# Performance work log

Hardware: AMD Instinct MI355X
Metric: run time of the kernel (lower is better)

The kernel has to match this reference:

```python
import jax, jax.numpy as jnp
import numpy as np

N_ORDER = 256      # HiPPO order (window_size=[256])
OUT_LEN = 96       # output_window_size
IN_LEN = 720       # input_window_size
MULTISCALE = [1, 2, 4]
MODES = 32         # min(32, min(OUT_LEN, IN_LEN)//2)
EPS = 1e-5


def _transition(N):
    Q = np.arange(N, dtype=np.float64)
    R = (2 * Q + 1)[:, None]
    j, i = np.meshgrid(Q, Q)
    A = np.where(i < j, -1.0, (-1.0) ** (i - j + 1)) * R
    B = (-1.0) ** Q[:, None] * R
    return A, B


def _bilinear_discretize(A, B, dt):
    # scipy cont2discrete(method='bilinear'): Ad = (I - dt/2 A)^-1 (I + dt/2 A), Bd = (I - dt/2 A)^-1 dt B
    n = A.shape[0]
    I = np.eye(n)
    ima = I - 0.5 * dt * A
    Ad = np.linalg.solve(ima, I + 0.5 * dt * A)
    Bd = np.linalg.solve(ima, dt * B)
    return Ad, Bd.squeeze(-1)


def _eval_legendre(N, x):
    # Legendre P_n(x), n=0..N-1, via three-term recurrence. Returns [len(x), N].
    P = np.zeros((N, x.shape[0]))
    P[0] = 1.0
    if N > 1:
        P[1] = x
    for n in range(1, N - 1):
        P[n + 1] = ((2 * n + 1) * x * P[n] - n * P[n - 1]) / (n + 1)
    return P.T


def setup_inputs() -> dict:
    key = jax.random.key(0)
    ks = jax.random.split(key, 4)
    B, L, E = 16, IN_LEN, 64
    x = jax.random.normal(ks[0], (B, L, E), dtype=jnp.float32)
    scale = 1.0 / (N_ORDER * N_ORDER)
    wr = scale * jax.random.uniform(ks[1], (3, N_ORDER, N_ORDER, MODES), dtype=jnp.float32)
    wi = scale * jax.random.uniform(ks[2], (3, N_ORDER, N_ORDER, MODES), dtype=jnp.float32)
    mlp_w = 0.1 * jax.random.normal(ks[3], (1, 3), dtype=jnp.float32)
    mlp_b = jnp.zeros((1,), dtype=jnp.float32)
    A_c, B_c = _transition(N_ORDER)
    Ads, Bds, evs = [], [], []
    for m in MULTISCALE:
        dt = 1.0 / OUT_LEN / m
        Ad, Bd = _bilinear_discretize(A_c, B_c, dt)
        vals = np.arange(0.0, 1.0, dt)
        ev = _eval_legendre(N_ORDER, 1.0 - 2.0 * vals)  # [m*OUT_LEN, N]
        Ads.append(Ad); Bds.append(Bd); evs.append(ev[-OUT_LEN:])
    A = jnp.asarray(np.stack(Ads), dtype=jnp.float32)          # [3,N,N]
    Bv = jnp.asarray(np.stack(Bds), dtype=jnp.float32)         # [3,N]
    eval_last = jnp.asarray(np.stack(evs), dtype=jnp.float32)  # [3,OUT_LEN,N]
    return {"x": x, "wr": wr, "wi": wi, "mlp_w": mlp_w, "mlp_b": mlp_b,
            "A": A, "Bv": Bv, "eval_last": eval_last}


def _hippo(xin, Ad, Bd):
    # xin: [B,E,T] -> states [B,E,N,T]; c_t = A c_{t-1} + B f_t
    c0 = jnp.zeros(xin.shape[:2] + (Ad.shape[0],), xin.dtype)
    def step(c, f):  # f: [B,E]
        c = c @ Ad.T + f[..., None] * Bd
        return c, c
    _, cs = jax.lax.scan(step, c0, jnp.moveaxis(xin, -1, 0))  # [T,B,E,N]
    return jnp.transpose(cs, (1, 2, 3, 0))


def _spec_conv(xc, wr, wi):
    # xc: [B,E,N,T]; FFT -> low-mode complex channel mix -> iFFT
    T = xc.shape[-1]
    x_ft = jnp.fft.rfft(xc)                 # [B,E,N,T//2+1]
    a = x_ft[..., :MODES]
    w = (wr + 1j * wi).astype(a.dtype)      # [N,N,MODES]
    out = jnp.einsum('bjix,iox->bjox', a, w)
    nf = T // 2 + 1
    out_ft = jnp.pad(out, ((0, 0), (0, 0), (0, 0), (0, nf - MODES)))
    return jnp.fft.irfft(out_ft, n=T)       # [B,E,N,T]


def reference(x, wr, wi, mlp_w, mlp_b, A, Bv, eval_last):
    # instance standard scale (RevIN-style, no affine)
    mean = jnp.mean(x, axis=1, keepdims=True)            # [B,1,E]
    std = jnp.sqrt(jnp.var(x, axis=1, keepdims=True) + EPS)
    xn = (x - mean) / std
    xe = jnp.transpose(xn, (0, 2, 1))                    # [B,E,L]
    decs = []
    for s, m in enumerate(MULTISCALE):
        T = m * OUT_LEN
        x_in = xe[:, :, -T:]
        xc = _hippo(x_in, A[s], Bv[s])                   # [B,E,N,T]
        out1 = _spec_conv(xc, wr[s], wi[s])              # [B,E,N,T]
        x_dec_c = out1[:, :, :, OUT_LEN - 1]             # [B,E,N]  (input >= output branch, jump_dist=0)
        decs.append(x_dec_c @ eval_last[s].T)            # [B,E,OUT_LEN]
    xd = jnp.stack(decs, axis=-1)                        # [B,E,OUT,3]
    xd = (xd @ mlp_w.T + mlp_b)[..., 0]                  # [B,E,OUT]
    xd = jnp.transpose(xd, (0, 2, 1))                    # [B,OUT,E]
    return xd * std + mean
```

## Files before the change

### kernel.cpp

```cpp
#include <hip/hip_runtime.h>

typedef unsigned short u16;
typedef unsigned int u32;

typedef __bf16 bf16x8 __attribute__((ext_vector_type(8)));
typedef unsigned short ushort8 __attribute__((ext_vector_type(8)));
typedef float f32x16 __attribute__((ext_vector_type(16)));

#define STATSP 2048
#define EPOFF 32768
#define KKOFF0 591872
#define KKOFF1 616448
#define KKOFF2 665600
#define WOFF 763904
#define R0OFF 5482496
#define R1OFF 6072320
#define R2OFF 7251968
#define HTOTOFF 11675648
#define AD64 0
#define PD64 196608
#define KKD64 589824

__device__ __forceinline__ u32 pack_hl(float a) {
  u32 bits = __builtin_bit_cast(u32, a);
  u32 hi = (bits + 0x7fffu + ((bits >> 16) & 1u)) >> 16;
  float hif = __builtin_bit_cast(float, hi << 16);
  float r = a - hif;
  u32 lo = __builtin_bit_cast(u32, r) >> 16;
  return hi | (lo << 16);
}

__device__ __forceinline__ void unpk8(const u32* p, bf16x8& h, bf16x8& l) {
  ushort8 hu, lu;
#pragma unroll
  for (int j = 0; j < 8; ++j) {
    u32 v = p[j];
    hu[j] = (unsigned short)(v & 0xffffu);
    lu[j] = (unsigned short)(v >> 16);
  }
  h = __builtin_bit_cast(bf16x8, hu);
  l = __builtin_bit_cast(bf16x8, lu);
}

__global__ __launch_bounds__(256) void k_pre(const float* __restrict__ Ab,
                                             const float* __restrict__ Bb,
                                             const float* __restrict__ xin,
                                             const float* __restrict__ ev,
                                             float* __restrict__ ws) {
  __shared__ float rs[4][64], rq[4][64];
  int blk = blockIdx.x, tid = threadIdx.x;
  if (blk < 771) {
    double* dws = (double*)(ws + WOFF);
    int idx = blk * 256 + tid;
    if (idx < 196608) {
      dws[AD64 + idx] = (double)Ab[idx];
    } else {
      int g = idx - 196608;
      const int rowoff[3] = {0, 24576, 73728};
      const int kko[3] = {KKOFF0, KKOFF1, KKOFF2};
      int s = g >> 8, i = g & 255;
      float v = Bb[g];
      dws[KKD64 + rowoff[s] + i] = (double)v;
      ((u32*)ws)[kko[s] + i] = pack_hl(v);
    }
  } else if (blk < 963) {
    int b2 = blk - 771;
    int b = b2 / 12, part = b2 % 12;
    int j = tid & 63, g = tid >> 6;
    const float* xp = xin + ((size_t)b * 720 + part * 60 + g) * 64 + j;
    float sum = 0.f, ss = 0.f;
#pragma unroll
    for (int i = 0; i < 15; ++i) {
      float v = xp[(size_t)i * 256];
      sum += v; ss += v * v;
    }
    rs[g][j] = sum; rq[g][j] = ss;
    __syncthreads();
    if (g == 0) {
      float s = rs[0][j] + rs[1][j] + rs[2][j] + rs[3][j];
      float q = rq[0][j] + rq[1][j] + rq[2][j] + rq[3][j];
      float* dst = ws + STATSP + ((size_t)b2 * 64 + j) * 2;
      dst[0] = s; dst[1] = q;
    }
  } else if (blk < 987) {
    int idx = (blk - 963) * 256 + tid;
    for (; idx < 36864; idx += 24 * 256) ws[HTOTOFF + idx] = 0.f;
  } else {
    int idx = (blk - 987) * 256 + tid;
    ((u32*)ws)[EPOFF + idx] = pack_hl(ev[idx]);
  }
}

struct G64Jobs {
  const double* A[8]; const double* B[8]; double* C[8]; float* CF[8];
  int M[8]; int transB[8]; int tile0[8];
  int njobs;
};

__global__ __launch_bounds__(256) void k_gemm64(G64Jobs jb) {
  int bid = blockIdx.x;
  int j = 0;
  for (int q = 1; q < jb.njobs; ++q) if (bid >= jb.tile0[q]) j = q;
  int local = bid - jb.tile0[j];
  int tm = local >> 3, tn = local & 7;
  const double* A = jb.A[j];
  const double* Bm = jb.B[j];
  double* C = jb.C[j];
  float* CF = jb.CF[j];
  int M = jb.M[j], tB = jb.transB[j];
  int row0 = tm * 32, col0 = tn * 32;
  __shared__ double As[32][33], Bs[32][33];
  int tid = threadIdx.x;
  int ty = tid >> 4, tx = tid & 15;
  int lr = tid >> 3, lk = (tid & 7) << 2;
  double va[4], vb[4];
#pragma unroll
  for (int u = 0; u < 4; ++u) {
    va[u] = (row0 + lr < M) ? A[(size_t)(row0 + lr) * 256 + lk + u] : 0.0;
    vb[u] = tB ? Bm[(size_t)(col0 + lr) * 256 + lk + u]
               : Bm[(size_t)lr * 256 + col0 + lk + u];
  }
  double a00 = 0., a01 = 0., a10 = 0., a11 = 0.;
  for (int kc = 0; kc < 256; kc += 32) {
#pragma unroll
    for (int u = 0; u < 4; ++u) {
      As[lr][lk + u] = va[u];
      if (tB) Bs[lk + u][lr] = vb[u];
      else    Bs[lr][lk + u] = vb[u];
    }
    __syncthreads();
    if (kc < 224) {
      int kn = kc + 32;
#pragma unroll
      for (int u = 0; u < 4; ++u) {
        va[u] = (row0 + lr < M) ? A[(size_t)(row0 + lr) * 256 + kn + lk + u] : 0.0;
        vb[u] = tB ? Bm[(size_t)(col0 + lr) * 256 + kn + lk + u]
                   : Bm[(size_t)(kn + lr) * 256 + col0 + lk + u];
      }
    }
#pragma unroll 8
    for (int k = 0; k < 32; ++k) {
      double x0 = As[2 * ty][k], x1 = As[2 * ty + 1][k];
      double y0 = Bs[k][2 * tx], y1 = Bs[k][2 * tx + 1];
      a00 = fma(x0, y0, a00); a01 = fma(x0, y1, a01);
      a10 = fma(x1, y0, a10); a11 = fma(x1, y1, a11);
    }
    __syncthreads();
  }
  int r0 = row0 + 2 * ty, c0 = col0 + 2 * tx;
  if (r0 < M) {
    C[(size_t)r0 * 256 + c0] = a00; C[(size_t)r0 * 256 + c0 + 1] = a01;
    if (CF) {
      ((u32*)CF)[(size_t)r0 * 256 + c0] = pack_hl((float)a00);
      ((u32*)CF)[(size_t)r0 * 256 + c0 + 1] = pack_hl((float)a01);
    }
  }
  if (r0 + 1 < M) {
    C[(size_t)(r0 + 1) * 256 + c0] = a10; C[(size_t)(r0 + 1) * 256 + c0 + 1] = a11;
    if (CF) {
      ((u32*)CF)[(size_t)(r0 + 1) * 256 + c0] = pack_hl((float)a10);
      ((u32*)CF)[(size_t)(r0 + 1) * 256 + c0 + 1] = pack_hl((float)a11);
    }
  }
}

__global__ __launch_bounds__(256) void k_s3(const float* __restrict__ wr,
                                            const float* __restrict__ wi,
                                            float* __restrict__ ws) {
  __shared__ u32 smem[6400];
  int bid = blockIdx.x;
  int jidx = bid >> 7;
  int r127 = bid & 127;
  int mb = ((r127 & 7) << 4) | (r127 >> 3);
  int s = jidx >> 1, p = jidx & 1;
  const float* w = (p ? wi : wr) + (size_t)s * 2097152;
  const u32* ep = (const u32*)ws + EPOFF + s * 24576;
  int i0 = mb * 2;
  int tid = threadIdx.x;
  int lane = tid & 63;
  int wid = tid >> 6;
  int il = wid & 1, kh = wid >> 1;

  int sh = tid >> 7;
  int sil = (tid >> 6) & 1;
  int so = (tid >> 1) & 31;
  int sx = (tid & 1) << 4;
  const float* wsrc = w + (((size_t)(i0 + sil) * 256 + sh * 128 + so) << 5) + sx;
  u32 sdst = sh * 2176 + (sil * 32 + sx) * 34 + so;

  int tcol = lane & 31;
  int og8 = (lane >> 5) << 3;
  const u32* asrc = smem + kh * 2176 + (il * 32 + tcol) * 34 + og8;
  const u32* bsrc = ep + tcol * 256 + og8;

  f32x16 acc[3];
#pragma unroll
  for (int f = 0; f < 3; ++f)
#pragma unroll
    for (int r = 0; r < 16; ++r) acc[f][r] = 0.f;

  float4 va0 = *(const float4*)(wsrc);
  float4 va1 = *(const float4*)(wsrc + 4);
  float4 va2 = *(const float4*)(wsrc + 8);
  float4 va3 = *(const float4*)(wsrc + 12);

  for (int c = 0; c < 4; ++c) {
    __syncthreads();
    {
      float vv[16] = {va0.x, va0.y, va0.z, va0.w, va1.x, va1.y, va1.z, va1.w,
                      va2.x, va2.y, va2.z, va2.w, va3.x, va3.y, va3.z, va3.w};
#pragma unroll
      for (int u = 0; u < 16; ++u) smem[sdst + u * 34] = pack_hl(vv[u]);
    }
    __syncthreads();
    if (c < 3) {
      const float* nsrc = wsrc + (size_t)(c + 1) * 1024;
      va0 = *(const float4*)(nsrc);
      va1 = *(const float4*)(nsrc + 4);
      va2 = *(const float4*)(nsrc + 8);
      va3 = *(const float4*)(nsrc + 12);
    }
    int ko = kh * 128 + c * 32;
#pragma unroll
    for (int ks = 0; ks < 2; ++ks) {
      const uint2* aq = (const uint2*)(asrc + ks * 16);
      uint2 q0 = aq[0], q1 = aq[1], q2 = aq[2], q3 = aq[3];
      u32 ap[8] = {q0.x, q0.y, q1.x, q1.y, q2.x, q2.y, q3.x, q3.y};
      bf16x8 ah, al;
      unpk8(ap, ah, al);
#pragma unroll
      for (int f = 0; f < 3; ++f) {
        const uint4* bq = (const uint4*)(bsrc + f * 8192 + ko + ks * 16);
        uint4 b0 = bq[0], b1 = bq[1];
        u32 bp[8] = {b0.x, b0.y, b0.z, b0.w, b1.x, b1.y, b1.z, b1.w};
        bf16x8 bh, bl;
        unpk8(bp, bh, bl);
        acc[f] = __builtin_amdgcn_mfma_f32_32x32x16_bf16(ah, bh, acc[f], 0, 0, 0);
        acc[f] = __builtin_amdgcn_mfma_f32_32x32x16_bf16(ah, bl, acc[f], 0, 0, 0);
        acc[f] = __builtin_amdgcn_mfma_f32_32x32x16_bf16(al, bh, acc[f], 0, 0, 0);
      }
    }
  }

  __syncthreads();
  float* ms = (float*)smem;
  int crow0 = (lane >> 5) << 2;
  if (kh == 1) {
#pragma unroll
    for (int f = 0; f < 3; ++f)
#pragma unroll
      for (int r = 0; r < 16; ++r) {
        int row = il * 32 + crow0 + (r & 3) + ((r >> 2) << 3);
        ms[row * 97 + f * 32 + tcol] = acc[f][r];
      }
  }
  __syncthreads();
  if (kh == 0) {
#pragma unroll
    for (int f = 0; f < 3; ++f)
#pragma unroll
      for (int r = 0; r < 16; ++r) {
        int row = il * 32 + crow0 + (r & 3) + ((r >> 2) << 3);
        int a = row * 97 + f * 32 + tcol;
        ms[a] += acc[f][r];
      }
  }
  __syncthreads();
  u32* W2 = (u32*)(ws + WOFF) + (size_t)jidx * 786432 + (size_t)(mb >> 2) * 24576 +
            ((mb & 3) << 1);
  int x = tid & 31, cg = tid >> 5;
#pragma unroll
  for (int j = 0; j < 12; ++j) {
    int c = cg * 12 + j;
    float v0 = ms[x * 97 + c];
    float v1 = ms[(32 + x) * 97 + c];
    uint2 st;
    st.x = pack_hl(v0);
    st.y = pack_hl(v1);
    *(uint2*)(W2 + (size_t)(x * 96 + c) * 8) = st;
  }
}

__global__ __launch_bounds__(256) void k_s4(float* __restrict__ ws) {
  int bid = blockIdx.x;
  const int cums[6] = {0, 36, 72, 144, 216, 360};
  int jidx = 0;
#pragma unroll
  for (int q = 1; q < 6; ++q) if (bid >= cums[q]) jidx = q;
  int local = bid - cums[jidx];
  int s = jidx >> 1, p = jidx & 1;
  const int Ts[3] = {96, 192, 384};
  const int KKo[3] = {KKOFF0, KKOFF1, KKOFF2};
  const int Ro[3] = {R0OFF, R1OFF, R2OFF};
  int T = Ts[s];
  int td = local / 12, tn = local % 12;
  int d0 = td * 32;
  int tid = threadIdx.x;
  int lane = tid & 63, wid = tid >> 6;
  int n0 = tn * 256 + wid * 64;
  int l31 = lane & 31, kg = lane >> 5;
  const u32* Ap = (const u32*)ws + KKo[s] + (size_t)(d0 + l31) * 256 + kg * 8;
  const u32* Bp = (const u32*)ws + WOFF + (size_t)jidx * 786432 + (size_t)kg * 24576;
  const u32* b0p = Bp + (size_t)(n0 + l31) * 8;
  const u32* b1p = Bp + (size_t)(n0 + 32 + l31) * 8;
  float* C = ws + Ro[s] + (size_t)p * T * 3072;

  f32x16 acc0, acc1;
#pragma unroll
  for (int r = 0; r < 16; ++r) { acc0[r] = 0.f; acc1[r] = 0.f; }

#pragma unroll 2
  for (int ks = 0; ks < 16; ++ks) {
    uint4 a0 = *(const uint4*)(Ap + ks * 16);
    uint4 a1 = *(const uint4*)(Ap + ks * 16 + 4);
    size_t bo = (size_t)ks * 49152;
    uint4 x0 = *(const uint4*)(b0p + bo);
    uint4 x1 = *(const uint4*)(b0p + bo + 4);
    uint4 y0 = *(const uint4*)(b1p + bo);
    uint4 y1 = *(const uint4*)(b1p + bo + 4);
    u32 ap[8] = {a0.x, a0.y, a0.z, a0.w, a1.x, a1.y, a1.z, a1.w};
    bf16x8 ah, al;
    unpk8(ap, ah, al);
    {
      u32 bp[8] = {x0.x, x0.y, x0.z, x0.w, x1.x, x1.y, x1.z, x1.w};
      bf16x8 bh, bl;
      unpk8(bp, bh, bl);
      acc0 = __builtin_amdgcn_mfma_f32_32x32x16_bf16(ah, bh, acc0, 0, 0, 0);
      acc0 = __builtin_amdgcn_mfma_f32_32x32x16_bf16(ah, bl, acc0, 0, 0, 0);
      acc0 = __builtin_amdgcn_mfma_f32_32x32x16_bf16(al, bh, acc0, 0, 0, 0);
      acc0 = __builtin_amdgcn_mfma_f32_32x32x16_bf16(al, bl, acc0, 0, 0, 0);
    }
    {
      u32 bp[8] = {y0.x, y0.y, y0.z, y0.w, y1.x, y1.y, y1.z, y1.w};
      bf16x8 bh, bl;
      unpk8(bp, bh, bl);
      acc1 = __builtin_amdgcn_mfma_f32_32x32x16_bf16(ah, bh, acc1, 0, 0, 0);
      acc1 = __builtin_amdgcn_mfma_f32_32x32x16_bf16(ah, bl, acc1, 0, 0, 0);
      acc1 = __builtin_amdgcn_mfma_f32_32x32x16_bf16(al, bh, acc1, 0, 0, 0);
      acc1 = __builtin_amdgcn_mfma_f32_32x32x16_bf16(al, bl, acc1, 0, 0, 0);
    }
  }

  int crow = kg << 2;
#pragma unroll
  for (int r = 0; r < 16; ++r) {
    int row = d0 + crow + (r & 3) + ((r >> 2) << 3);
    C[(size_t)row * 3072 + n0 + l31] = acc0[r];
    C[(size_t)row * 3072 + n0 + 32 + l31] = acc1[r];
  }
}

__global__ __launch_bounds__(192) void k_s5a(const float* __restrict__ mlpw, float* __restrict__ ws) {
  int bid = blockIdx.x;
  int s = bid >> 7;
  int rem = bid & 127;
  int x = rem >> 2;
  int tq = rem & 3;
  const int Ts[3] = {96, 192, 384};
  const int Ro[3] = {R0OFF, R1OFF, R2OFF};
  const int lpbase[3] = {288, 192, 0};
  int T = Ts[s];
  int Lc = T >> 3;
  __shared__ float cs[384][2];
  __shared__ float Lsr[8][24], Lsi[8][24];
  int tid = threadIdx.x;
  for (int e = tid; e < T; e += 192) {
    float th = 6.283185307179586f * (float)e / (float)T;
    cs[e][0] = cosf(th);
    cs[e][1] = sinf(th);
  }
  int c = tid / 24, tl = tid % 24;
  int t = tq * 24 + tl;
  const float* Rre = ws + Ro[s] + (size_t)x * 96 + t;
  const float* Rim = Rre + (size_t)T * 3072;
  float* Htot = ws + HTOTOFF;
  float wsc = mlpw[s];
  __syncthreads();
  int d0 = c * Lc;
  float zr = 0.f, zi = 0.f;
  for (int d = d0; d < d0 + Lc; ++d) {
    float rr = Rre[(size_t)d * 3072];
    float ri = Rim[(size_t)d * 3072];
    int e1 = (x * d) % T;
    float c1 = cs[e1][0], s1 = cs[e1][1];
    zr += c1 * rr + s1 * ri;
    zi += c1 * ri - s1 * rr;
  }
  Lsr[c][tl] = zr; Lsi[c][tl] = zi;
  __syncthreads();
  if (c == 0) {
    float pr = 0.f, pi = 0.f;
#pragma unroll
    for (int cc = 0; cc < 8; ++cc) {
      float lr = Lsr[cc][tl], li = Lsi[cc][tl];
      Lsr[cc][tl] = pr; Lsi[cc][tl] = pi;
      pr += lr; pi += li;
    }
  }
  __syncthreads();
  zr = Lsr[c][tl]; zi = Lsi[c][tl];
  float sc = (((x == 0) ? 1.f : 2.f) / (float)T) * wsc;
  for (int d = d0; d < d0 + Lc; ++d) {
    float rr = Rre[(size_t)d * 3072];
    float ri = Rim[(size_t)d * 3072];
    int e1 = (x * d) % T;
    float c1 = cs[e1][0], s1 = cs[e1][1];
    zr += c1 * rr + s1 * ri;
    zi += c1 * ri - s1 * rr;
    int k = T - 1 - d;
    int e2 = (x * (95 - k)) % T;
    if (e2 < 0) e2 += T;
    float c2 = cs[e2][0], s2 = cs[e2][1];
    atomicAdd(Htot + (size_t)(lpbase[s] + k) * 96 + t, sc * (c2 * zr - s2 * zi));
  }
}

__global__ __launch_bounds__(256) void k_s6(const float* __restrict__ xin, const float* __restrict__ mlpb_p,
                                            const float* __restrict__ ws, float* __restrict__ out) {
  int b = blockIdx.x >> 2, tq = blockIdx.x & 3;
  int tid = threadIdx.x;
  int j = tid & 63, tsub = tid >> 6;
  __shared__ float Ht[384 * 24];
  for (int idx = tid; idx < 384 * 24; idx += 256) {
    int lp = idx / 24, c = idx % 24;
    Ht[idx] = ws[HTOTOFF + lp * 96 + tq * 24 + c];
  }
  float ssum = 0.f, sq = 0.f;
#pragma unroll
  for (int p = 0; p < 12; ++p) {
    const float* src = ws + STATSP + (((size_t)b * 12 + p) * 64 + j) * 2;
    ssum += src[0]; sq += src[1];
  }
  float mn = ssum * (1.f / 720.f);
  float var = sq * (1.f / 720.f) - mn * mn;
  float sd = sqrtf(var + 1e-5f);
  __syncthreads();
  float mlpb = mlpb_p[0];
  float acc[6] = {0.f, 0.f, 0.f, 0.f, 0.f, 0.f};
  float accS[6] = {0.f, 0.f, 0.f, 0.f, 0.f, 0.f};
  const float* xp = xin + ((size_t)b * 720 + 336) * 64 + j;
  for (int lp = 0; lp < 384; ++lp) {
    float xv = xp[(size_t)lp * 64];
    const float* hr = &Ht[lp * 24 + tsub * 6];
    float2 h01 = *(const float2*)&hr[0];
    float2 h23 = *(const float2*)&hr[2];
    float2 h45 = *(const float2*)&hr[4];
    float hh[6] = {h01.x, h01.y, h23.x, h23.y, h45.x, h45.y};
#pragma unroll
    for (int u = 0; u < 6; ++u) {
      acc[u] += xv * hh[u];
      accS[u] += hh[u];
    }
  }
#pragma unroll
  for (int u = 0; u < 6; ++u) {
    int t = tq * 24 + tsub * 6 + u;
    float val = acc[u] + mn * (1.f - accS[u]) + sd * mlpb;
    out[((size_t)b * 96 + t) * 64 + j] = val;
  }
}

extern "C" void kernel_launch(void* const* d_in, const int* in_sizes, int n_in,
                              void* d_out, int out_size, void* d_ws, size_t ws_size,
                              hipStream_t stream) {
  const float* x  = (const float*)d_in[0];
  const float* wr = (const float*)d_in[1];
  const float* wi = (const float*)d_in[2];
  const float* mw = (const float*)d_in[3];
  const float* mb = (const float*)d_in[4];
  const float* Ab = (const float*)d_in[5];
  const float* Bb = (const float*)d_in[6];
  const float* ev = (const float*)d_in[7];
  float* wsf = (float*)d_ws;
  float* out = (float*)d_out;

  k_pre<<<1275, 256, 0, stream>>>(Ab, Bb, x, ev, wsf);

  const double* AD = (const double*)(wsf + WOFF) + AD64;
  double* PD = (double*)(wsf + WOFF) + PD64;
  double* KD = (double*)(wsf + WOFF) + KKD64;
  static const int Ts[3] = {96, 192, 384};
  static const int rowoff[3] = {0, 24576, 73728};
  static const int KKo[3] = {KKOFF0, KKOFF1, KKOFF2};

  int have[3] = {1, 1, 1};
  for (int r = 0; r <= 8; ++r) {
    G64Jobs jb;
    jb.njobs = 0;
    int tiles = 0;
    for (int s = 0; s < 3; ++s) {
      int T = Ts[s];
      if (have[s] >= T) continue;
      const double* Pn = (r == 0) ? (AD + (size_t)s * 65536)
                                  : (PD + (size_t)(2 * s + (r & 1)) * 65536);
      int M = ((2 * have[s] < T) ? 2 * have[s] : T) - have[s];
      int q = jb.njobs++;
      jb.A[q] = KD + rowoff[s]; jb.B[q] = Pn;
      jb.C[q] = KD + rowoff[s] + (size_t)have[s] * 256;
      jb.CF[q] = wsf + KKo[s] + (size_t)have[s] * 256;
      jb.M[q] = M; jb.transB[q] = 1; jb.tile0[q] = tiles;
      tiles += ((M + 31) / 32) * 8;
      if (2 * have[s] < T) {
        q = jb.njobs++;
        jb.A[q] = Pn; jb.B[q] = Pn;
        jb.C[q] = PD + (size_t)(2 * s + ((r + 1) & 1)) * 65536;
        jb.CF[q] = nullptr;
        jb.M[q] = 256; jb.transB[q] = 0; jb.tile0[q] = tiles;
        tiles += 64;
      }
      have[s] = (2 * have[s] < T) ? 2 * have[s] : T;
    }
    if (jb.njobs) k_gemm64<<<tiles, 256, 0, stream>>>(jb);
  }

  k_s3<<<768, 256, 0, stream>>>(wr, wi, wsf);
  k_s4<<<504, 256, 0, stream>>>(wsf);
  k_s5a<<<384, 192, 0, stream>>>(mw, wsf);
  k_s6<<<64, 256, 0, stream>>>(x, mb, wsf, out);
}
```

Baseline: 374.2 us.

## Load k_s3 weight operands directly from global instead of staging through LDS

Kernel k_s3 stops staging the fp32 weight tile through shared memory with double syncs per chunk. Each lane now reads its A-fragment elements straight from global memory (strided 32 floats apart, coalesced across lanes on the mode index) and packs them into bf16 hi/lo in registers. Shared memory shrinks to just the reduction buffer, and launch bounds request 3 blocks per CU to raise occupancy. The trade-off is that the software prefetch across chunks is lost, so load latency must be hidden by occupancy and the partial unroll instead.

```diff
diff --git a/kernel.cpp b/kernel.cpp
--- a/kernel.cpp
+++ b/kernel.cpp
@@ -164,10 +164,10 @@
   }
 }
 
-__global__ __launch_bounds__(256) void k_s3(const float* __restrict__ wr,
-                                            const float* __restrict__ wi,
-                                            float* __restrict__ ws) {
-  __shared__ u32 smem[6400];
+__global__ __launch_bounds__(256, 3) void k_s3(const float* __restrict__ wr,
+                                               const float* __restrict__ wi,
+                                               float* __restrict__ ws) {
+  __shared__ float ms[64 * 97];
   int bid = blockIdx.x;
   int jidx = bid >> 7;
   int r127 = bid & 127;
@@ -181,16 +181,9 @@
   int wid = tid >> 6;
   int il = wid & 1, kh = wid >> 1;
 
-  int sh = tid >> 7;
-  int sil = (tid >> 6) & 1;
-  int so = (tid >> 1) & 31;
-  int sx = (tid & 1) << 4;
-  const float* wsrc = w + (((size_t)(i0 + sil) * 256 + sh * 128 + so) << 5) + sx;
-  u32 sdst = sh * 2176 + (sil * 32 + sx) * 34 + so;
-
   int tcol = lane & 31;
   int og8 = (lane >> 5) << 3;
-  const u32* asrc = smem + kh * 2176 + (il * 32 + tcol) * 34 + og8;
+  const float* aw0 = w + (((size_t)(i0 + il) * 256 + kh * 128 + og8) << 5) + tcol;
   const u32* bsrc = ep + tcol * 256 + og8;
 
   f32x16 acc[3];
@@ -199,33 +192,15 @@
 #pragma unroll
     for (int r = 0; r < 16; ++r) acc[f][r] = 0.f;
 
-  float4 va0 = *(const float4*)(wsrc);
-  float4 va1 = *(const float4*)(wsrc + 4);
-  float4 va2 = *(const float4*)(wsrc + 8);
-  float4 va3 = *(const float4*)(wsrc + 12);
-
+#pragma unroll 2
   for (int c = 0; c < 4; ++c) {
-    __syncthreads();
-    {
-      float vv[16] = {va0.x, va0.y, va0.z, va0.w, va1.x, va1.y, va1.z, va1.w,
-                      va2.x, va2.y, va2.z, va2.w, va3.x, va3.y, va3.z, va3.w};
-#pragma unroll
-      for (int u = 0; u < 16; ++u) smem[sdst + u * 34] = pack_hl(vv[u]);
-    }
-    __syncthreads();
-    if (c < 3) {
-      const float* nsrc = wsrc + (size_t)(c + 1) * 1024;
-      va0 = *(const float4*)(nsrc);
-      va1 = *(const float4*)(nsrc + 4);
-      va2 = *(const float4*)(nsrc + 8);
-      va3 = *(const float4*)(nsrc + 12);
-    }
     int ko = kh * 128 + c * 32;
 #pragma unroll
     for (int ks = 0; ks < 2; ++ks) {
-      const uint2* aq = (const uint2*)(asrc + ks * 16);
-      uint2 q0 = aq[0], q1 = aq[1], q2 = aq[2], q3 = aq[3];
-      u32 ap[8] = {q0.x, q0.y, q1.x, q1.y, q2.x, q2.y, q3.x, q3.y};
+      const float* aw = aw0 + ((c * 32 + ks * 16) << 5);
+      u32 ap[8];
+#pragma unroll
+      for (int j2 = 0; j2 < 8; ++j2) ap[j2] = pack_hl(aw[(size_t)j2 << 5]);
       bf16x8 ah, al;
       unpk8(ap, ah, al);
 #pragma unroll
@@ -242,8 +217,6 @@
     }
   }
 
-  __syncthreads();
-  float* ms = (float*)smem;
   int crow0 = (lane >> 5) << 2;
   if (kh == 1) {
 #pragma unroll
```

Measured after the change: 376.7 us. No clear change (+0.7%).
